# Kernel tuning notes

Hardware: AMD Instinct MI355X
Metric: run time of the kernel (lower is better)

## Reference

```python
import jax, jax.numpy as jnp
import numpy as np

EMBED_DIM = 512
NUM_HEADS = 8
HEAD_DIM = EMBED_DIM // NUM_HEADS
B, N, M = 4, 4096, 4096


def setup_inputs() -> dict:
    key = jax.random.key(0)
    ks = jax.random.split(key, 16)
    s = 0.02
    inp = {
        "query": jax.random.normal(ks[0], (B, N, EMBED_DIM), jnp.float32),
        "key": jax.random.normal(ks[1], (B, M, EMBED_DIM), jnp.float32),
        "value": jax.random.normal(ks[2], (B, M, EMBED_DIM), jnp.float32),
        # Linear weights stored as (in, out) so y = x @ W + b (== torch x @ W.T + b)
        "Wq": jax.random.normal(ks[3], (EMBED_DIM, EMBED_DIM), jnp.float32) * s,
        "bq": jnp.zeros((EMBED_DIM,), jnp.float32),
        "Wk": jax.random.normal(ks[4], (EMBED_DIM, EMBED_DIM), jnp.float32) * s,
        "bk": jnp.zeros((EMBED_DIM,), jnp.float32),
        "Wv": jax.random.normal(ks[5], (EMBED_DIM, EMBED_DIM), jnp.float32) * s,
        "bv": jnp.zeros((EMBED_DIM,), jnp.float32),
        # rank expansion MLP acts per-head on head_dim
        "W1": jax.random.normal(ks[6], (HEAD_DIM, HEAD_DIM * 2), jnp.float32) * s,
        "b1": jnp.zeros((HEAD_DIM * 2,), jnp.float32),
        "W2": jax.random.normal(ks[7], (HEAD_DIM * 2, HEAD_DIM), jnp.float32) * s,
        "b2": jnp.zeros((HEAD_DIM,), jnp.float32),
        "Wo": jax.random.normal(ks[8], (EMBED_DIM, EMBED_DIM), jnp.float32) * s,
        "bo": jnp.zeros((EMBED_DIM,), jnp.float32),
    }
    return inp


def reference(query, key, value, Wq, bq, Wk, bk, Wv, bv, W1, b1, W2, b2, Wo, bo):
    b, n, _ = query.shape
    m = key.shape[1]
    H, D = NUM_HEADS, HEAD_DIM
    # ELU+1 feature maps on projected q, k
    q = jax.nn.elu(query @ Wq + bq) + 1.0           # [B,N,E]
    k = jax.nn.elu(key @ Wk + bk) + 1.0             # [B,M,E]
    v = value @ Wv + bv                              # [B,M,E]
    q = q.reshape(b, n, H, D)
    k = k.reshape(b, m, H, D)
    v = v.reshape(b, m, H, D)
    # rank expansion MLP on keys (per head_dim), exact GELU as nn.GELU default
    k_aug = jax.nn.gelu(k @ W1 + b1, approximate=False) @ W2 + b2
    k_aug = jax.nn.elu(k_aug) + 1.0                  # [B,M,H,D]
    # inputs already fp32 (torch .float() casts are identity here)
    k_scaled = k_aug / m                             # normalize over context len
    kv_context = jnp.einsum('bmhd,bmhe->bhde', k_scaled, v)   # [B,H,D,D]
    out = jnp.einsum('bnhd,bhde->bnhe', q, kv_context)        # [B,N,H,D]
    k_sum = k_scaled.sum(axis=1)                      # [B,H,D]
    denom = jnp.einsum('bnhd,bhd->bnh', q, k_sum)     # [B,N,H]
    out = out / jnp.clip(denom, 1e-6, None)[..., None]
    out = jnp.clip(jnp.nan_to_num(out, nan=0.0, posinf=65000.0, neginf=-65000.0),
                   -65000.0, 65000.0)
    out = out.reshape(b, n, H * D)
    return out @ Wo + bo
```

## Files before the change

### kernel.cpp

```cpp
#include <hip/hip_runtime.h>
#include <cmath>

#define DEV __device__ __forceinline__

typedef __bf16 bf16x8 __attribute__((ext_vector_type(8)));
typedef float f32x4 __attribute__((ext_vector_type(4)));
typedef unsigned int u32;
typedef unsigned short u16;

DEV u16 f2bf(float f) {
  union { float f; u32 u; } v;
  v.f = f;
  u32 u = v.u;
  u += 0x7fffu + ((u >> 16) & 1u);
  return (u16)(u >> 16);
}
DEV __bf16 bfbits(u16 b) {
  union { u16 u; __bf16 h; } v;
  v.u = b;
  return v.h;
}

DEV void async16(const void* g, void* l) {
  __builtin_amdgcn_global_load_lds((const __attribute__((address_space(1))) u32*)g,
                                   (__attribute__((address_space(3))) u32*)l, 16, 0, 0);
}

enum { ACT_ID = 0, ACT_ELU1 = 1, ACT_GELU = 2, ACT_ELU1S = 3 };
enum { OM_ROW = 0, OM_VT = 1 };

DEV float apply_act(int ACT, float v, float scale) {
  if (ACT == ACT_ELU1)  return (v > 0.f) ? (v + 1.f) : __expf(v);
  if (ACT == ACT_GELU)  return 0.5f * v * (1.f + erff(v * 0.7071067811865475f));
  if (ACT == ACT_ELU1S) return ((v > 0.f) ? (v + 1.f) : __expf(v)) * scale;
  return v;
}

template <int BM, int BN, int K, int WR, int WC, int ACT, int OBF16, int OMODE, int AFP32>
__global__ __launch_bounds__(256)
void gemm_bf16(const void* __restrict__ Av, const u16* __restrict__ Bt,
               const float* __restrict__ bias, void* __restrict__ Yv,
               int NC, float scale)
{
  constexpr int AI = AFP32 ? BM / 32 : BM / 64;
  constexpr int BI = BN / 64;
  constexpr int ABYTES = AFP32 ? BM * 128 : BM * 64;
  __shared__ __align__(16) char AsRaw[ABYTES];
  __shared__ u16 Bs[BN * 32];
  static_assert(WR * WC == 4, "4 waves");

  const int tid = threadIdx.x;
  const int wv = tid >> 6, lane = tid & 63;
  const int wr = wv / WC, wc = wv % WC;
  const int lrow = lane & 15, lq = lane >> 4;
  const int c0 = blockIdx.x * BN;
  const long r0 = (long)blockIdx.y * BM;
  const float* Af = (const float*)Av;
  const u16* Ah = (const u16*)Av;

  f32x4 acc[4][4] = {};

  for (int kt = 0; kt < K; kt += 32) {
    if (AFP32) {
#pragma unroll
      for (int i = 0; i < AI; ++i) {
        const int s = (wv * AI + i) * 64 + lane;
        const int row = s >> 3, p = s & 7;
        const int gp = p ^ (row & 7);
        async16(Af + (r0 + row) * K + kt + gp * 4, AsRaw + (wv * AI + i) * 1024);
      }
    } else {
#pragma unroll
      for (int i = 0; i < AI; ++i) {
        const int s = (wv * AI + i) * 64 + lane;
        async16(Ah + (r0 + (s >> 2)) * (long)K + kt + (s & 3) * 8,
                AsRaw + (wv * AI + i) * 1024);
      }
    }
#pragma unroll
    for (int i = 0; i < BI; ++i) {
      const int s = (wv * BI + i) * 64 + lane;
      async16(Bt + ((long)c0 + (s >> 2)) * K + kt + (s & 3) * 8,
              (char*)Bs + (wv * BI + i) * 1024);
    }
    __syncthreads();
    bf16x8 af[4], bfr[4];
#pragma unroll
    for (int i = 0; i < 4; ++i) {
      const int r = wr * 64 + i * 16 + lrow;
      if (AFP32) {
        const float* Asf = (const float*)AsRaw;
        const int r7 = r & 7, P0 = lq * 2;
        float4 lo = *(const float4*)&Asf[r * 32 + (P0 ^ r7) * 4];
        float4 hi = *(const float4*)&Asf[r * 32 + ((P0 + 1) ^ r7) * 4];
        af[i][0] = bfbits(f2bf(lo.x)); af[i][1] = bfbits(f2bf(lo.y));
        af[i][2] = bfbits(f2bf(lo.z)); af[i][3] = bfbits(f2bf(lo.w));
        af[i][4] = bfbits(f2bf(hi.x)); af[i][5] = bfbits(f2bf(hi.y));
        af[i][6] = bfbits(f2bf(hi.z)); af[i][7] = bfbits(f2bf(hi.w));
      } else {
        af[i] = *(const bf16x8*)((const u16*)AsRaw + r * 32 + lq * 8);
      }
    }
#pragma unroll
    for (int j = 0; j < 4; ++j)
      bfr[j] = *(const bf16x8*)&Bs[(wc * 64 + j * 16 + lrow) * 32 + lq * 8];
#pragma unroll
    for (int i = 0; i < 4; ++i)
#pragma unroll
      for (int j = 0; j < 4; ++j)
        acc[i][j] = __builtin_amdgcn_mfma_f32_16x16x32_bf16(af[i], bfr[j], acc[i][j], 0, 0, 0);
    __syncthreads();
  }

  float* Yf = (float*)Yv;
  u16* Yh = (u16*)Yv;
#pragma unroll
  for (int i = 0; i < 4; ++i) {
#pragma unroll
    for (int j = 0; j < 4; ++j) {
      const int col = c0 + wc * 64 + j * 16 + lrow;
      const float bv = bias[col];
      float o[4];
#pragma unroll
      for (int p = 0; p < 4; ++p) o[p] = apply_act(ACT, acc[i][j][p] + bv, scale);

      if (OMODE == OM_ROW) {
#pragma unroll
        for (int p = 0; p < 4; ++p) {
          const long row = r0 + wr * 64 + i * 16 + lq * 4 + p;
          const long yi = row * NC + col;
          if (OBF16) Yh[yi] = f2bf(o[p]);
          else       Yf[yi] = o[p];
        }
      } else {
        const int b = (int)(r0 >> 12);
        const int m = (int)(r0 & 4095) + wr * 64 + i * 16 + lq * 4;
        const int h = col >> 6, e = col & 63;
        ushort4 w;
        w.x = f2bf(o[0]); w.y = f2bf(o[1]); w.z = f2bf(o[2]); w.w = f2bf(o[3]);
        *(ushort4*)(Yh + (((long)b * 8 + h) * 64 + e) * 4096 + m) = w;
      }
    }
  }
}

struct TArgs {
  const float* src[6];
  u16* dst[6];
  int K[6];
  int N[6];
};
__global__ __launch_bounds__(256)
void transpose_w(TArgs a)
{
  const int m = blockIdx.z;
  const int K = a.K[m], N = a.N[m];
  const int kt = blockIdx.y * 64, nt = blockIdx.x * 64;
  if (kt >= K || nt >= N) return;
  const float* src = a.src[m];
  u16* dst = a.dst[m];
  __shared__ u16 t[64][72];
  const int tx = threadIdx.x & 15, ty = threadIdx.x >> 4;
#pragma unroll
  for (int rr = 0; rr < 64; rr += 16) {
    const int k = kt + ty + rr;
    float4 v = *(const float4*)(src + (long)k * N + nt + tx * 4);
    t[tx * 4 + 0][ty + rr] = f2bf(v.x);
    t[tx * 4 + 1][ty + rr] = f2bf(v.y);
    t[tx * 4 + 2][ty + rr] = f2bf(v.z);
    t[tx * 4 + 3][ty + rr] = f2bf(v.w);
  }
  __syncthreads();
#pragma unroll
  for (int it = 0; it < 2; ++it) {
    const int s = threadIdx.x + it * 256;
    const int r = s >> 3, c = (s & 7) * 8;
    ushort4 u0 = *(ushort4*)&t[r][c];
    ushort4 u1 = *(ushort4*)&t[r][c + 4];
    *(ushort4*)(dst + (long)(nt + r) * K + kt + c) = u0;
    *(ushort4*)(dst + (long)(nt + r) * K + kt + c + 4) = u1;
  }
}

__global__ __launch_bounds__(256)
void mlp_fused(const u16* __restrict__ kact, const u16* __restrict__ W1T,
               const u16* __restrict__ W2T, const float* __restrict__ b1,
               const float* __restrict__ b2, u16* __restrict__ kaT, float invM)
{
  __shared__ __align__(16) u16 SB[27136];
  u16* As  = SB;
  u16* W1p = SB + 9216;
  u16* W2p = SB + 18432;
  u16* hid = SB;

  const int tid = threadIdx.x, wv = tid >> 6, lane = tid & 63;
  const int lrow = lane & 15, lq = lane >> 4;
  const int bh = blockIdx.y, b = bh >> 3, h = bh & 7;
  const int m0 = blockIdx.x * 128;
  const long kbase = ((long)b * 4096 + m0) * 512 + h * 64;

#pragma unroll
  for (int i = 0; i < 4; ++i) {
    const int c = i * 256 + tid;
    const int row = c >> 3, p = c & 7;
    uint4 v = *(const uint4*)(kact + kbase + (long)row * 512 + p * 8);
    *(uint4*)&As[row * 72 + p * 8] = v;
  }
#pragma unroll
  for (int i = 0; i < 4; ++i) {
    const int c = i * 256 + tid;
    const int row = c >> 3, p = c & 7;
    uint4 v = *(const uint4*)(W1T + c * 8);
    *(uint4*)&W1p[row * 72 + p * 8] = v;
  }
#pragma unroll
  for (int i = 0; i < 4; ++i) {
    const int c = i * 256 + tid;
    const int row = c >> 4, p = c & 15;
    uint4 v = *(const uint4*)(W2T + c * 8);
    *(uint4*)&W2p[row * 136 + p * 8] = v;
  }
  __syncthreads();

  const int c0 = (wv >> 1) * 64, mh0 = (wv & 1) * 64;
  f32x4 acc1[4][4] = {};
#pragma unroll
  for (int kt = 0; kt < 2; ++kt) {
    bf16x8 wa[4], kb[4];
#pragma unroll
    for (int i = 0; i < 4; ++i)
      wa[i] = *(const bf16x8*)&W1p[(c0 + i * 16 + lrow) * 72 + kt * 32 + lq * 8];
#pragma unroll
    for (int j = 0; j < 4; ++j)
      kb[j] = *(const bf16x8*)&As[(mh0 + j * 16 + lrow) * 72 + kt * 32 + lq * 8];
#pragma unroll
    for (int i = 0; i < 4; ++i)
#pragma unroll
      for (int j = 0; j < 4; ++j)
        acc1[i][j] = __builtin_amdgcn_mfma_f32_16x16x32_bf16(wa[i], kb[j], acc1[i][j], 0, 0, 0);
  }
  __syncthreads();

#pragma unroll
  for (int i = 0; i < 4; ++i) {
    const int cc = c0 + i * 16 + lq * 4;
    float4 bv = *(const float4*)(b1 + cc);
#pragma unroll
    for (int j = 0; j < 4; ++j) {
      const int m = mh0 + j * 16 + lrow;
      float x0 = acc1[i][j][0] + bv.x, x1 = acc1[i][j][1] + bv.y;
      float x2 = acc1[i][j][2] + bv.z, x3 = acc1[i][j][3] + bv.w;
      ushort4 w;
      w.x = f2bf(0.5f * x0 * (1.f + erff(x0 * 0.7071067811865475f)));
      w.y = f2bf(0.5f * x1 * (1.f + erff(x1 * 0.7071067811865475f)));
      w.z = f2bf(0.5f * x2 * (1.f + erff(x2 * 0.7071067811865475f)));
      w.w = f2bf(0.5f * x3 * (1.f + erff(x3 * 0.7071067811865475f)));
      *(ushort4*)&hid[m * 136 + cc] = w;
    }
  }
  __syncthreads();

  const int d0 = (wv >> 1) * 32, mh2 = (wv & 1) * 64;
  f32x4 acc2[2][4] = {};
#pragma unroll
  for (int kt = 0; kt < 4; ++kt) {
    bf16x8 wa[2], hb[4];
#pragma unroll
    for (int i = 0; i < 2; ++i)
      wa[i] = *(const bf16x8*)&W2p[(d0 + i * 16 + lrow) * 136 + kt * 32 + lq * 8];
#pragma unroll
    for (int j = 0; j < 4; ++j)
      hb[j] = *(const bf16x8*)&hid[(mh2 + j * 16 + lrow) * 136 + kt * 32 + lq * 8];
#pragma unroll
    for (int i = 0; i < 2; ++i)
#pragma unroll
      for (int j = 0; j < 4; ++j)
        acc2[i][j] = __builtin_amdgcn_mfma_f32_16x16x32_bf16(wa[i], hb[j], acc2[i][j], 0, 0, 0);
  }

#pragma unroll
  for (int i = 0; i < 2; ++i) {
    const int dd = d0 + i * 16 + lq * 4;
    float4 bv = *(const float4*)(b2 + dd);
    float bva[4] = {bv.x, bv.y, bv.z, bv.w};
#pragma unroll
    for (int j = 0; j < 4; ++j) {
      const int m = m0 + mh2 + j * 16 + lrow;
#pragma unroll
      for (int p = 0; p < 4; ++p) {
        float v = acc2[i][j][p] + bva[p];
        v = ((v > 0.f) ? (v + 1.f) : __expf(v)) * invM;
        kaT[((long)bh * 64 + dd + p) * 4096 + m] = f2bf(v);
      }
    }
  }
}

__global__ __launch_bounds__(256)
void kv_gemm(const u16* __restrict__ kaT, const u16* __restrict__ vT,
             float* __restrict__ kvp, float* __restrict__ ksp)
{
  const int sp = blockIdx.x;
  const int bh = blockIdx.y;
  __shared__ u16 SB[16384];
  u16* As = SB;
  u16* Bs = SB + 8192;
  const int tid = threadIdx.x, wv = tid >> 6, lane = tid & 63;
  const int lrow = lane & 15, lq = lane >> 4;
  f32x4 acc[4][4] = {};
  f32x4 accs[4] = {};
  bf16x8 ones;
#pragma unroll
  for (int z = 0; z < 8; ++z) ones[z] = (__bf16)1.0f;
  const long base = (long)bh * 64 * 4096;

  for (int ph = 0; ph < 2; ++ph) {
    const int m0 = sp * 256 + ph * 128;
#pragma unroll
    for (int i = 0; i < 4; ++i) {
      const int s = (wv * 4 + i) * 64 + lane;
      const int chunk = s >> 8, row = (s >> 2) & 63, part = s & 3;
      const long g = base + (long)row * 4096 + m0 + chunk * 32 + part * 8;
      async16(kaT + g, &As[(wv * 4 + i) * 512]);
      async16(vT + g, &Bs[(wv * 4 + i) * 512]);
    }
    __syncthreads();
    bf16x8 af[4], bfr[4];
#pragma unroll
    for (int i = 0; i < 4; ++i)
      af[i] = *(const bf16x8*)&As[wv * 2048 + (i * 16 + lrow) * 32 + lq * 8];
#pragma unroll
    for (int j = 0; j < 4; ++j)
      bfr[j] = *(const bf16x8*)&Bs[wv * 2048 + (j * 16 + lrow) * 32 + lq * 8];
#pragma unroll
    for (int i = 0; i < 4; ++i) {
#pragma unroll
      for (int j = 0; j < 4; ++j)
        acc[i][j] = __builtin_amdgcn_mfma_f32_16x16x32_bf16(af[i], bfr[j], acc[i][j], 0, 0, 0);
      accs[i] = __builtin_amdgcn_mfma_f32_16x16x32_bf16(af[i], ones, accs[i], 0, 0, 0);
    }
    __syncthreads();
  }

  float* red = (float*)SB;
  float* ksr = red + 64 * 68;
  for (int w = 0; w < 4; ++w) {
    __syncthreads();
    if (wv == w) {
#pragma unroll
      for (int i = 0; i < 4; ++i) {
#pragma unroll
        for (int j = 0; j < 4; ++j) {
          const int e = j * 16 + lrow, dd = i * 16 + lq * 4;
          float* p = &red[e * 68 + dd];
          if (w == 0) { p[0] = acc[i][j][0]; p[1] = acc[i][j][1]; p[2] = acc[i][j][2]; p[3] = acc[i][j][3]; }
          else        { p[0] += acc[i][j][0]; p[1] += acc[i][j][1]; p[2] += acc[i][j][2]; p[3] += acc[i][j][3]; }
        }
        if (lrow == 0) {
          const int dd = i * 16 + lq * 4;
#pragma unroll
          for (int p2 = 0; p2 < 4; ++p2) {
            if (w == 0) ksr[dd + p2] = accs[i][p2];
            else        ksr[dd + p2] += accs[i][p2];
          }
        }
      }
    }
  }
  __syncthreads();
  float* kvo = kvp + ((long)sp * 32 + bh) * 4096;
  for (int s = tid; s < 4096; s += 256) kvo[s] = red[(s >> 6) * 68 + (s & 63)];
  if (tid < 64) ksp[(sp * 32 + bh) * 64 + tid] = ksr[tid];
}

__global__ __launch_bounds__(256)
void kv_reduce(const float* __restrict__ kvp, const float* __restrict__ ksp,
               u16* __restrict__ kvT, u16* __restrict__ ksumT)
{
  const int bh = blockIdx.x;
  const int t = threadIdx.x;
  for (int s = t; s < 4096; s += 256) {
    float v = 0.f;
#pragma unroll
    for (int sp = 0; sp < 16; ++sp) v += kvp[((long)sp * 32 + bh) * 4096 + s];
    kvT[(long)bh * 4096 + s] = f2bf(v);
  }
  if (t < 64) {
    float v = 0.f;
#pragma unroll
    for (int sp = 0; sp < 16; ++sp) v += ksp[(sp * 32 + bh) * 64 + t];
    ksumT[bh * 64 + t] = f2bf(v);
  }
}

__global__ __launch_bounds__(256)
void attn_mfma(const u16* __restrict__ q, const u16* __restrict__ kvT,
               const u16* __restrict__ ksumT, u16* __restrict__ attn)
{
  __shared__ u16 SB[17408];
  const int tid = threadIdx.x, wv = tid >> 6, lane = tid & 63;
  const int lrow = lane & 15, lq = lane >> 4;
  const int n0 = blockIdx.x * 256;
  const int bh = blockIdx.y, b = bh >> 3, h = bh & 7;
  u16* As = SB;

#pragma unroll
  for (int half = 0; half < 2; ++half)
#pragma unroll
    for (int i = 0; i < 4; ++i) {
      const int s = (wv * 4 + i) * 64 + lane;
      async16(q + ((long)(b * 4096 + n0 + (s >> 2))) * 512 + h * 64 + half * 32 + (s & 3) * 8,
              &As[half * 8192 + (wv * 4 + i) * 512]);
    }
  bf16x8 bfr[2][4], ks[2];
#pragma unroll
  for (int half = 0; half < 2; ++half) {
#pragma unroll
    for (int j = 0; j < 4; ++j)
      bfr[half][j] = *(const bf16x8*)(kvT + ((long)bh * 64 + j * 16 + lrow) * 64 + half * 32 + lq * 8);
    ks[half] = *(const bf16x8*)(ksumT + bh * 64 + half * 32 + lq * 8);
  }
  __syncthreads();

  f32x4 acc[4][4] = {};
  f32x4 accd[4] = {};
#pragma unroll
  for (int half = 0; half < 2; ++half) {
    bf16x8 af[4];
#pragma unroll
    for (int i = 0; i < 4; ++i)
      af[i] = *(const bf16x8*)&As[half * 8192 + (wv * 64 + i * 16 + lrow) * 32 + lq * 8];
#pragma unroll
    for (int i = 0; i < 4; ++i) {
#pragma unroll
      for (int j = 0; j < 4; ++j)
        acc[i][j] = __builtin_amdgcn_mfma_f32_16x16x32_bf16(af[i], bfr[half][j], acc[i][j], 0, 0, 0);
      accd[i] = __builtin_amdgcn_mfma_f32_16x16x32_bf16(af[i], ks[half], accd[i], 0, 0, 0);
    }
  }
  __syncthreads();

  u16* LT = SB;
#pragma unroll
  for (int i = 0; i < 4; ++i) {
    float dinv[4];
#pragma unroll
    for (int p = 0; p < 4; ++p) dinv[p] = 1.f / fmaxf(accd[i][p], 1e-6f);
#pragma unroll
    for (int j = 0; j < 4; ++j) {
      const int e = j * 16 + lrow;
      const int nl0 = i * 16 + lq * 4;
      ushort4 w;
      float x0 = acc[i][j][0] * dinv[0], x1 = acc[i][j][1] * dinv[1];
      float x2 = acc[i][j][2] * dinv[2], x3 = acc[i][j][3] * dinv[3];
      if (!(x0 == x0)) x0 = 0.f;
      if (!(x1 == x1)) x1 = 0.f;
      if (!(x2 == x2)) x2 = 0.f;
      if (!(x3 == x3)) x3 = 0.f;
      w.x = f2bf(fminf(65000.f, fmaxf(-65000.f, x0)));
      w.y = f2bf(fminf(65000.f, fmaxf(-65000.f, x1)));
      w.z = f2bf(fminf(65000.f, fmaxf(-65000.f, x2)));
      w.w = f2bf(fminf(65000.f, fmaxf(-65000.f, x3)));
      *(ushort4*)&LT[wv * 4352 + e * 68 + nl0] = w;
    }
  }
  __syncthreads();
#pragma unroll
  for (int it = 0; it < 8; ++it) {
    const int c = it * 256 + tid;
    const int n = c & 255, ec = c >> 8;
    const int wr2 = n >> 6, nl = n & 63;
    ushort4 w0, w1;
    w0.x = LT[wr2 * 4352 + (ec * 8 + 0) * 68 + nl];
    w0.y = LT[wr2 * 4352 + (ec * 8 + 1) * 68 + nl];
    w0.z = LT[wr2 * 4352 + (ec * 8 + 2) * 68 + nl];
    w0.w = LT[wr2 * 4352 + (ec * 8 + 3) * 68 + nl];
    w1.x = LT[wr2 * 4352 + (ec * 8 + 4) * 68 + nl];
    w1.y = LT[wr2 * 4352 + (ec * 8 + 5) * 68 + nl];
    w1.z = LT[wr2 * 4352 + (ec * 8 + 6) * 68 + nl];
    w1.w = LT[wr2 * 4352 + (ec * 8 + 7) * 68 + nl];
    u16* dst = attn + ((long)(b * 4096 + n0 + n)) * 512 + h * 64 + ec * 8;
    *(ushort4*)dst = w0;
    *(ushort4*)(dst + 4) = w1;
  }
}

static constexpr long U = 8388608;

extern "C" void kernel_launch(void* const* d_in, const int* in_sizes, int n_in,
                              void* d_out, int out_size, void* d_ws, size_t ws_size,
                              hipStream_t stream)
{
  const float* query = (const float*)d_in[0];
  const float* key   = (const float*)d_in[1];
  const float* value = (const float*)d_in[2];
  const float* Wq = (const float*)d_in[3];
  const float* bq = (const float*)d_in[4];
  const float* Wk = (const float*)d_in[5];
  const float* bk = (const float*)d_in[6];
  const float* Wv = (const float*)d_in[7];
  const float* bv = (const float*)d_in[8];
  const float* W1 = (const float*)d_in[9];
  const float* b1 = (const float*)d_in[10];
  const float* W2 = (const float*)d_in[11];
  const float* b2 = (const float*)d_in[12];
  const float* Wo = (const float*)d_in[13];
  const float* bo = (const float*)d_in[14];

  u16* wsh = (u16*)d_ws;
  u16* qact = wsh;
  u16* kact = wsh + U;
  u16* vT   = wsh + 2 * U;
  u16* kaT  = wsh + 3 * U;
  u16* attn = wsh + 4 * U;

  float* fp  = (float*)(wsh + 5 * U);
  float* kvp = fp;
  float* ksp = fp + 2097152;
  u16* kvTg   = (u16*)(fp + 2129920);
  u16* ksumTg = kvTg + 131072;
  u16* wtb = ksumTg + 2048;
  u16* WqT = wtb;
  u16* WkT = wtb + 262144;
  u16* WvT = wtb + 524288;
  u16* WoT = wtb + 786432;
  u16* W1T = wtb + 1048576;
  u16* W2T = wtb + 1056768;

  dim3 blk(256);
  const float invM = 1.f / 4096.f;

  TArgs ta;
  ta.src[0] = Wq; ta.dst[0] = WqT; ta.K[0] = 512; ta.N[0] = 512;
  ta.src[1] = Wk; ta.dst[1] = WkT; ta.K[1] = 512; ta.N[1] = 512;
  ta.src[2] = Wv; ta.dst[2] = WvT; ta.K[2] = 512; ta.N[2] = 512;
  ta.src[3] = Wo; ta.dst[3] = WoT; ta.K[3] = 512; ta.N[3] = 512;
  ta.src[4] = W1; ta.dst[4] = W1T; ta.K[4] = 64;  ta.N[4] = 128;
  ta.src[5] = W2; ta.dst[5] = W2T; ta.K[5] = 128; ta.N[5] = 64;
  transpose_w<<<dim3(8, 8, 6), blk, 0, stream>>>(ta);

  gemm_bf16<128,128,512,2,2,ACT_ELU1,1,OM_ROW,1><<<dim3(4,128), blk, 0, stream>>>(query, WqT, bq, qact, 512, 1.f);
  gemm_bf16<128,128,512,2,2,ACT_ELU1,1,OM_ROW,1><<<dim3(4,128), blk, 0, stream>>>(key,   WkT, bk, kact, 512, 1.f);
  gemm_bf16<128,128,512,2,2,ACT_ID,  1,OM_VT, 1><<<dim3(4,128), blk, 0, stream>>>(value, WvT, bv, vT,   512, 1.f);
  mlp_fused<<<dim3(32,32), blk, 0, stream>>>(kact, W1T, W2T, b1, b2, kaT, invM);
  kv_gemm<<<dim3(16,32), blk, 0, stream>>>(kaT, vT, kvp, ksp);
  kv_reduce<<<dim3(32), blk, 0, stream>>>(kvp, ksp, kvTg, ksumTg);
  attn_mfma<<<dim3(16,32), blk, 0, stream>>>(qact, kvTg, ksumTg, attn);
  gemm_bf16<128,128,512,2,2,ACT_ID,0,OM_ROW,0><<<dim3(4,128), blk, 0, stream>>>(attn, WoT, bo, (float*)d_out, 512, 1.f);
}
```

Measured before the change: 295.3 us.

## Convert fp32 A to bf16 at load and stage transposed outputs through LDS

The fp32-input GEMM path now loads A with plain vector global reads and converts it to bf16 before storing to shared memory. This halves the LDS footprint and removes the per-tile conversion from the fragment reads, but gives up the async global-to-LDS copy. The transposed-V epilogue and the MLP kaT output now write tiles into LDS first, then issue coalesced 16-byte global stores, replacing scattered 8-byte or 2-byte stores. The LDS staging adds barriers and shared-memory traffic in exchange for better global write coalescing.

```diff
diff --git a/kernel.cpp b/kernel.cpp
--- a/kernel.cpp
+++ b/kernel.cpp
@@ -15,11 +15,6 @@
   u += 0x7fffu + ((u >> 16) & 1u);
   return (u16)(u >> 16);
 }
-DEV __bf16 bfbits(u16 b) {
-  union { u16 u; __bf16 h; } v;
-  v.u = b;
-  return v.h;
-}
 
 DEV void async16(const void* g, void* l) {
   __builtin_amdgcn_global_load_lds((const __attribute__((address_space(1))) u32*)g,
@@ -42,11 +37,12 @@
                const float* __restrict__ bias, void* __restrict__ Yv,
                int NC, float scale)
 {
-  constexpr int AI = AFP32 ? BM / 32 : BM / 64;
   constexpr int BI = BN / 64;
-  constexpr int ABYTES = AFP32 ? BM * 128 : BM * 64;
-  __shared__ __align__(16) char AsRaw[ABYTES];
-  __shared__ u16 Bs[BN * 32];
+  constexpr int SBASE = BM * 32 + BN * 32;
+  constexpr int SBSZ = (OMODE == OM_VT && 4 * 64 * 72 > SBASE) ? 4 * 64 * 72 : SBASE;
+  __shared__ __align__(16) u16 SB[SBSZ];
+  u16* AsU = SB;
+  u16* Bs = SB + BM * 32;
   static_assert(WR * WC == 4, "4 waves");
 
   const int tid = threadIdx.x;
@@ -62,45 +58,39 @@
 
   for (int kt = 0; kt < K; kt += 32) {
     if (AFP32) {
-#pragma unroll
-      for (int i = 0; i < AI; ++i) {
-        const int s = (wv * AI + i) * 64 + lane;
-        const int row = s >> 3, p = s & 7;
-        const int gp = p ^ (row & 7);
-        async16(Af + (r0 + row) * K + kt + gp * 4, AsRaw + (wv * AI + i) * 1024);
+      const int row = tid >> 2, kq = tid & 3;
+#pragma unroll
+      for (int it = 0; it < BM / 64; ++it) {
+        const int r = it * 64 + row;
+        const float* g = Af + (r0 + r) * K + kt + kq * 8;
+        float4 lo = *(const float4*)g;
+        float4 hi = *(const float4*)(g + 4);
+        union { ushort4 h[2]; uint4 q; } pk;
+        pk.h[0].x = f2bf(lo.x); pk.h[0].y = f2bf(lo.y);
+        pk.h[0].z = f2bf(lo.z); pk.h[0].w = f2bf(lo.w);
+        pk.h[1].x = f2bf(hi.x); pk.h[1].y = f2bf(hi.y);
+        pk.h[1].z = f2bf(hi.z); pk.h[1].w = f2bf(hi.w);
+        *(uint4*)&AsU[r * 32 + kq * 8] = pk.q;
       }
     } else {
 #pragma unroll
-      for (int i = 0; i < AI; ++i) {
-        const int s = (wv * AI + i) * 64 + lane;
+      for (int i = 0; i < BM / 64; ++i) {
+        const int s = (wv * (BM / 64) + i) * 64 + lane;
         async16(Ah + (r0 + (s >> 2)) * (long)K + kt + (s & 3) * 8,
-                AsRaw + (wv * AI + i) * 1024);
+                &AsU[(wv * (BM / 64) + i) * 512]);
       }
     }
 #pragma unroll
     for (int i = 0; i < BI; ++i) {
       const int s = (wv * BI + i) * 64 + lane;
       async16(Bt + ((long)c0 + (s >> 2)) * K + kt + (s & 3) * 8,
-              (char*)Bs + (wv * BI + i) * 1024);
+              &Bs[(wv * BI + i) * 512]);
     }
     __syncthreads();
     bf16x8 af[4], bfr[4];
 #pragma unroll
-    for (int i = 0; i < 4; ++i) {
-      const int r = wr * 64 + i * 16 + lrow;
-      if (AFP32) {
-        const float* Asf = (const float*)AsRaw;
-        const int r7 = r & 7, P0 = lq * 2;
-        float4 lo = *(const float4*)&Asf[r * 32 + (P0 ^ r7) * 4];
-        float4 hi = *(const float4*)&Asf[r * 32 + ((P0 + 1) ^ r7) * 4];
-        af[i][0] = bfbits(f2bf(lo.x)); af[i][1] = bfbits(f2bf(lo.y));
-        af[i][2] = bfbits(f2bf(lo.z)); af[i][3] = bfbits(f2bf(lo.w));
-        af[i][4] = bfbits(f2bf(hi.x)); af[i][5] = bfbits(f2bf(hi.y));
-        af[i][6] = bfbits(f2bf(hi.z)); af[i][7] = bfbits(f2bf(hi.w));
-      } else {
-        af[i] = *(const bf16x8*)((const u16*)AsRaw + r * 32 + lq * 8);
-      }
-    }
+    for (int i = 0; i < 4; ++i)
+      af[i] = *(const bf16x8*)&AsU[(wr * 64 + i * 16 + lrow) * 32 + lq * 8];
 #pragma unroll
     for (int j = 0; j < 4; ++j)
       bfr[j] = *(const bf16x8*)&Bs[(wc * 64 + j * 16 + lrow) * 32 + lq * 8];
@@ -114,32 +104,51 @@
 
   float* Yf = (float*)Yv;
   u16* Yh = (u16*)Yv;
-#pragma unroll
-  for (int i = 0; i < 4; ++i) {
-#pragma unroll
-    for (int j = 0; j < 4; ++j) {
-      const int col = c0 + wc * 64 + j * 16 + lrow;
-      const float bv = bias[col];
-      float o[4];
-#pragma unroll
-      for (int p = 0; p < 4; ++p) o[p] = apply_act(ACT, acc[i][j][p] + bv, scale);
-
-      if (OMODE == OM_ROW) {
+
+  if (OMODE == OM_ROW) {
+#pragma unroll
+    for (int i = 0; i < 4; ++i) {
+#pragma unroll
+      for (int j = 0; j < 4; ++j) {
+        const int col = c0 + wc * 64 + j * 16 + lrow;
+        const float bv = bias[col];
 #pragma unroll
         for (int p = 0; p < 4; ++p) {
+          const float o = apply_act(ACT, acc[i][j][p] + bv, scale);
           const long row = r0 + wr * 64 + i * 16 + lq * 4 + p;
           const long yi = row * NC + col;
-          if (OBF16) Yh[yi] = f2bf(o[p]);
-          else       Yf[yi] = o[p];
+          if (OBF16) Yh[yi] = f2bf(o);
+          else       Yf[yi] = o;
         }
-      } else {
-        const int b = (int)(r0 >> 12);
-        const int m = (int)(r0 & 4095) + wr * 64 + i * 16 + lq * 4;
-        const int h = col >> 6, e = col & 63;
+      }
+    }
+  } else {
+    u16* LTv = SB + wv * 4608;
+#pragma unroll
+    for (int i = 0; i < 4; ++i) {
+#pragma unroll
+      for (int j = 0; j < 4; ++j) {
+        const int col = c0 + wc * 64 + j * 16 + lrow;
+        const float bv = bias[col];
         ushort4 w;
-        w.x = f2bf(o[0]); w.y = f2bf(o[1]); w.z = f2bf(o[2]); w.w = f2bf(o[3]);
-        *(ushort4*)(Yh + (((long)b * 8 + h) * 64 + e) * 4096 + m) = w;
+        w.x = f2bf(apply_act(ACT, acc[i][j][0] + bv, scale));
+        w.y = f2bf(apply_act(ACT, acc[i][j][1] + bv, scale));
+        w.z = f2bf(apply_act(ACT, acc[i][j][2] + bv, scale));
+        w.w = f2bf(apply_act(ACT, acc[i][j][3] + bv, scale));
+        const int e_l = j * 16 + lrow;
+        const int m_l = i * 16 + lq * 4;
+        *(ushort4*)&LTv[e_l * 72 + m_l] = w;
       }
+    }
+    const int b = (int)(r0 >> 12);
+    const int h = (c0 + wc * 64) >> 6;
+    const int mg0 = (int)(r0 & 4095) + wr * 64;
+#pragma unroll
+    for (int ps = 0; ps < 8; ++ps) {
+      const int e = ps * 8 + (lane >> 3);
+      const int mq = (lane & 7) * 8;
+      uint4 v = *(const uint4*)&LTv[e * 72 + mq];
+      *(uint4*)(Yh + (((long)b * 8 + h) * 64 + e) * 4096 + mg0 + mq) = v;
     }
   }
 }
@@ -192,6 +201,7 @@
   u16* W1p = SB + 9216;
   u16* W2p = SB + 18432;
   u16* hid = SB;
+  u16* LT2 = SB;
 
   const int tid = threadIdx.x, wv = tid >> 6, lane = tid & 63;
   const int lrow = lane & 15, lq = lane >> 4;
@@ -261,7 +271,7 @@
   __syncthreads();
 
   const int d0 = (wv >> 1) * 32, mh2 = (wv & 1) * 64;
-  f32x4 acc2[2][4] = {};
+  f32x4 acc2[4][2] = {};
 #pragma unroll
   for (int kt = 0; kt < 4; ++kt) {
     bf16x8 wa[2], hb[4];
@@ -272,27 +282,37 @@
     for (int j = 0; j < 4; ++j)
       hb[j] = *(const bf16x8*)&hid[(mh2 + j * 16 + lrow) * 136 + kt * 32 + lq * 8];
 #pragma unroll
-    for (int i = 0; i < 2; ++i)
-#pragma unroll
-      for (int j = 0; j < 4; ++j)
-        acc2[i][j] = __builtin_amdgcn_mfma_f32_16x16x32_bf16(wa[i], hb[j], acc2[i][j], 0, 0, 0);
-  }
+    for (int j = 0; j < 4; ++j)
+#pragma unroll
+      for (int i = 0; i < 2; ++i)
+        acc2[j][i] = __builtin_amdgcn_mfma_f32_16x16x32_bf16(hb[j], wa[i], acc2[j][i], 0, 0, 0);
+  }
+  __syncthreads();
 
 #pragma unroll
   for (int i = 0; i < 2; ++i) {
-    const int dd = d0 + i * 16 + lq * 4;
-    float4 bv = *(const float4*)(b2 + dd);
-    float bva[4] = {bv.x, bv.y, bv.z, bv.w};
+    const int d = d0 + i * 16 + lrow;
+    const float bd = b2[d];
 #pragma unroll
     for (int j = 0; j < 4; ++j) {
-      const int m = m0 + mh2 + j * 16 + lrow;
+      const int ml = mh2 + j * 16 + lq * 4;
+      ushort4 w;
 #pragma unroll
       for (int p = 0; p < 4; ++p) {
-        float v = acc2[i][j][p] + bva[p];
+        float v = acc2[j][i][p] + bd;
         v = ((v > 0.f) ? (v + 1.f) : __expf(v)) * invM;
-        kaT[((long)bh * 64 + dd + p) * 4096 + m] = f2bf(v);
+        ((u16*)&w)[p] = f2bf(v);
       }
-    }
+      *(ushort4*)&LT2[d * 136 + ml] = w;
+    }
+  }
+  __syncthreads();
+#pragma unroll
+  for (int it = 0; it < 4; ++it) {
+    const int c = it * 256 + tid;
+    const int d = c >> 4, mq = (c & 15) * 8;
+    uint4 v = *(const uint4*)&LT2[d * 136 + mq];
+    *(uint4*)(kaT + ((long)bh * 64 + d) * 4096 + m0 + mq) = v;
   }
 }
 
```

Result: slower. 305.9 us (+3.6%).
